# Kernel optimization log

Measured on AMD Instinct MI355X. Metric: run time of the kernel, lower is better.

Reference implementation:

```python
import jax, jax.numpy as jnp
import numpy as np

EPS = 1e-6
NHEADS = 16


def setup_inputs() -> dict:
    key = jax.random.key(0)
    ks = jax.random.split(key, 6)
    b, n, dim, h = 2, 2048, 2048, NHEADS
    d = dim // h
    x = jax.random.normal(ks[0], (b, n, dim), dtype=jnp.float32)
    qkv_w = jax.random.normal(ks[1], (3 * dim, dim), dtype=jnp.float32) * (dim ** -0.5)
    qkv_b = jax.random.normal(ks[2], (3 * dim,), dtype=jnp.float32) * 0.01
    q_norm_w = jnp.ones((d,), dtype=jnp.float32)
    k_norm_w = jnp.ones((d,), dtype=jnp.float32)
    # Flux-style rotation matrices: (1, 1, n, d/2, 2, 2)
    pos = jnp.arange(n, dtype=jnp.float32)[:, None]
    inv_freq = 1.0 / (10000.0 ** (jnp.arange(0, d, 2, dtype=jnp.float32) / d))  # [d/2]
    ang = pos * inv_freq[None, :]  # [n, d/2]
    cos, sin = jnp.cos(ang), jnp.sin(ang)
    rot = jnp.stack([jnp.stack([cos, -sin], axis=-1),
                     jnp.stack([sin, cos], axis=-1)], axis=-1)  # [n, d/2, 2, 2]
    rot = rot[None, None]  # [1,1,n,d/2,2,2]
    return {"x": x, "qkv_w": qkv_w, "qkv_b": qkv_b,
            "q_norm_w": q_norm_w, "k_norm_w": k_norm_w, "rot": rot}


def _rmsnorm(t, w):
    t32 = t.astype(jnp.float32)
    inv = jax.lax.rsqrt(jnp.mean(t32 * t32, axis=-1, keepdims=True) + EPS)
    return ((t32 * inv) * w).astype(t.dtype)


def _apply_rope(t, rot):
    # t: [b,h,n,d]; rot: [1,1,n,d/2,2,2]
    b, h, n, d = t.shape
    tx = t.astype(jnp.float32).reshape(b, h, n, d // 2, 1, 2)
    out = rot[..., 0] * tx[..., 0] + rot[..., 1] * tx[..., 1]  # [b,h,n,d/2,2]
    return out.reshape(b, h, n, d).astype(t.dtype)


def reference(x, qkv_w, qkv_b, q_norm_w, k_norm_w, rot):
    b, n, dim = x.shape
    d = q_norm_w.shape[0]
    h = dim // d
    qkv = x @ qkv_w.T + qkv_b  # [b, n, 3*dim]
    # layout per Rearrange 'b n (h d j) -> b h n d j'
    qkv = qkv.reshape(b, n, h, d, 3).transpose(0, 2, 1, 3, 4)  # [b,h,n,d,3]
    q, k, v = qkv[..., 0], qkv[..., 1], qkv[..., 2]
    q = _apply_rope(_rmsnorm(q, q_norm_w), rot)
    k = _apply_rope(_rmsnorm(k, k_norm_w), rot)
    scores = jnp.einsum('bhqd,bhkd->bhqk', q, k) * (d ** -0.5)
    attn = jax.nn.softmax(scores, axis=-1)
    out = jnp.einsum('bhqk,bhkd->bhqd', attn, v)
    return out.transpose(0, 2, 1, 3).reshape(b, n, dim)  # b n (h d)
```

## Files before the change

kernel.cpp:

```cpp
#include <hip/hip_runtime.h>
#include <cstdint>
#include <cstddef>


#define LOG2E 1.4426950408889634f
#define ATT_SCALE 0.08838834764831845f
#define QSCALE (ATT_SCALE * LOG2E)

typedef __attribute__((ext_vector_type(8))) __bf16 bf16x8;
typedef __attribute__((ext_vector_type(4))) __bf16 bf16x4;
typedef __attribute__((ext_vector_type(4))) float f32x4;

__device__ __forceinline__ float b2f(unsigned u) {
  u <<= 16;
  return __builtin_bit_cast(float, u);
}
__device__ __forceinline__ unsigned short f2b(float f) {
  unsigned x = __builtin_bit_cast(unsigned, f);
  return (unsigned short)((x + 0x7fffu + ((x >> 16) & 1u)) >> 16);
}
__device__ __forceinline__ void gl16(const void* g, void* l) {
  __builtin_amdgcn_global_load_lds((__attribute__((address_space(1))) void*)(g),
                                   (__attribute__((address_space(3))) void*)(l), 16, 0, 0);
}

__global__ void k_cvt(const float4* __restrict__ in, ushort4* __restrict__ out, int n4) {
  int i = blockIdx.x * blockDim.x + threadIdx.x;
  int st = gridDim.x * blockDim.x;
  for (; i < n4; i += st) {
    float4 v = in[i];
    ushort4 o;
    o.x = f2b(v.x); o.y = f2b(v.y); o.z = f2b(v.z); o.w = f2b(v.w);
    out[i] = o;
  }
}

__global__ __launch_bounds__(512, 2) void k_gemm(const unsigned short* __restrict__ A,
                                                 const unsigned short* __restrict__ W,
                                                 const float* __restrict__ bias,
                                                 unsigned short* __restrict__ C) {
  __shared__ __align__(16) unsigned short lds[65536];
  const int tid = threadIdx.x;
  const int w = tid >> 6, l = tid & 63;
  const int lo = l & 15, hi = l >> 4;
  const int WM = w >> 2, WN = w & 3;
  const int wg = blockIdx.x;
  const int swz = (wg & 7) * 64 + (wg >> 3);
  const int mbase = (swz >> 4) * 128, nbase = (swz & 15) * 384;

  const int srow = w * 16 + (l >> 2);
  const int scol = ((l & 3) * 8) ^ (((srow >> 1) & 3) << 3);

  auto stage = [&](int t, int slot) {
    unsigned short* Sa = lds + slot * 16384;
    unsigned short* Sb = Sa + 4096;
    const int kt = t * 32;
    gl16(A + (size_t)(mbase + srow) * 2048 + kt + scol,
         Sa + (w * 16) * 32);
#pragma unroll
    for (int rd = 0; rd < 3; ++rd)
      gl16(W + (size_t)(nbase + rd * 128 + srow) * 2048 + kt + scol,
           Sb + (rd * 128 + w * 16) * 32);
  };

  f32x4 acc[4][6] = {};
  stage(0, 0); stage(1, 1); stage(2, 2);

  const int ea = (hi * 8) ^ (((lo >> 1) & 3) << 3);
  for (int t = 0; t < 64; ++t) {
    if (t < 62)       asm volatile("s_waitcnt vmcnt(8) lgkmcnt(0)" ::: "memory");
    else if (t == 62) asm volatile("s_waitcnt vmcnt(4) lgkmcnt(0)" ::: "memory");
    else              asm volatile("s_waitcnt vmcnt(0) lgkmcnt(0)" ::: "memory");
    __builtin_amdgcn_sched_barrier(0);
    __builtin_amdgcn_s_barrier();
    __builtin_amdgcn_sched_barrier(0);
    if (t + 3 < 64) stage(t + 3, (t + 3) & 3);

    const unsigned short* Sa = lds + (t & 3) * 16384;
    const unsigned short* Sb = Sa + 4096;
    bf16x8 af[4], bf[6];
#pragma unroll
    for (int i = 0; i < 4; ++i)
      af[i] = *(const bf16x8*)&Sa[(WM * 64 + i * 16 + lo) * 32 + ea];
#pragma unroll
    for (int j = 0; j < 6; ++j)
      bf[j] = *(const bf16x8*)&Sb[(WN * 96 + j * 16 + lo) * 32 + ea];

    __builtin_amdgcn_s_setprio(1);
#pragma unroll
    for (int i = 0; i < 4; ++i)
#pragma unroll
      for (int j = 0; j < 6; ++j)
        acc[i][j] = __builtin_amdgcn_mfma_f32_16x16x32_bf16(af[i], bf[j], acc[i][j], 0, 0, 0);
    __builtin_amdgcn_s_setprio(0);
  }

  const int rowb = mbase + WM * 64;
  const int colb = nbase + WN * 96;
#pragma unroll
  for (int j = 0; j < 6; ++j) {
    float bj = bias[colb + j * 16 + lo];
#pragma unroll
    for (int i = 0; i < 4; ++i)
#pragma unroll
      for (int r = 0; r < 4; ++r) {
        int row = rowb + i * 16 + hi * 4 + r;
        C[(size_t)row * 6144 + colb + j * 16 + lo] = f2b(acc[i][j][r] + bj);
      }
  }
}

__global__ __launch_bounds__(256) void k_normrope(const unsigned short* __restrict__ qkv,
                                                  const float* __restrict__ qw,
                                                  const float* __restrict__ kw,
                                                  const float* __restrict__ rot,
                                                  unsigned short* __restrict__ Q,
                                                  unsigned short* __restrict__ K,
                                                  unsigned short* __restrict__ V) {
  const int l = threadIdx.x & 63;
  const int idx = blockIdx.x * 4 + (threadIdx.x >> 6);
  const int h = idx & 15;
  const int n = (idx >> 4) & 2047;
  const int b = idx >> 15;
  const unsigned* p = (const unsigned*)(qkv + (size_t)(b * 2048 + n) * 6144 + h * 384 + l * 6);
  unsigned u0 = p[0], u1 = p[1], u2 = p[2];
  float q0 = b2f(u0 & 0xffff), k0 = b2f(u0 >> 16);
  float v0 = b2f(u1 & 0xffff), q1 = b2f(u1 >> 16);
  float k1 = b2f(u2 & 0xffff), v1 = b2f(u2 >> 16);
  (void)v0; (void)v1;
  float sq = q0 * q0 + q1 * q1, sk = k0 * k0 + k1 * k1;
#pragma unroll
  for (int m = 1; m < 64; m <<= 1) {
    sq += __shfl_xor(sq, m, 64);
    sk += __shfl_xor(sk, m, 64);
  }
  float qi = rsqrtf(sq * (1.0f / 128.0f) + 1e-6f) * QSCALE;
  float ki = rsqrtf(sk * (1.0f / 128.0f) + 1e-6f);
  float2 qwv = *(const float2*)&qw[2 * l];
  float2 kwv = *(const float2*)&kw[2 * l];
  float4 r = *(const float4*)&rot[n * 256 + l * 4];
  float qn0 = q0 * qi * qwv.x, qn1 = q1 * qi * qwv.y;
  float kn0 = k0 * ki * kwv.x, kn1 = k1 * ki * kwv.y;
  unsigned qo = (unsigned)f2b(r.x * qn0 + r.y * qn1) | ((unsigned)f2b(r.z * qn0 + r.w * qn1) << 16);
  unsigned ko = (unsigned)f2b(r.x * kn0 + r.y * kn1) | ((unsigned)f2b(r.z * kn0 + r.w * kn1) << 16);
  unsigned vo = (u1 & 0xffffu) | (u2 & 0xffff0000u);
  size_t ob = ((size_t)(b * 16 + h) * 2048 + n) * 128 + 2 * l;
  *(unsigned*)(Q + ob) = qo;
  *(unsigned*)(K + ob) = ko;
  *(unsigned*)(V + ob) = vo;
}

__global__ __launch_bounds__(256) void k_transpose(const unsigned short* __restrict__ V,
                                                   unsigned short* __restrict__ Vt) {
  __shared__ unsigned short tile[64 * 66];
  const int t = threadIdx.x;
  const int d0 = blockIdx.x * 64;
  const int n0 = blockIdx.y * 64;
  const int bh = blockIdx.z;
#pragma unroll
  for (int s = t; s < 512; s += 256) {
    int nr = s >> 3, c8 = (s & 7) * 8;
    uint4 vv = *(const uint4*)(V + ((size_t)bh * 2048 + n0 + nr) * 128 + d0 + c8);
    unsigned* tp = (unsigned*)&tile[nr * 66 + c8];
    tp[0] = vv.x; tp[1] = vv.y; tp[2] = vv.z; tp[3] = vv.w;
  }
  __syncthreads();
#pragma unroll
  for (int s = t; s < 512; s += 256) {
    int dr = s >> 3, n8 = (s & 7) * 8;
    unsigned short e[8];
#pragma unroll
    for (int j = 0; j < 8; ++j) e[j] = tile[(n8 + j) * 66 + dr];
    uint4 o;
    o.x = e[0] | ((unsigned)e[1] << 16);
    o.y = e[2] | ((unsigned)e[3] << 16);
    o.z = e[4] | ((unsigned)e[5] << 16);
    o.w = e[6] | ((unsigned)e[7] << 16);
    *(uint4*)(Vt + ((size_t)bh * 128 + d0 + dr) * 2048 + n0 + n8) = o;
  }
}

__global__ __launch_bounds__(512, 4) void k_attn(const unsigned short* __restrict__ Q,
                                                 const unsigned short* __restrict__ K,
                                                 const unsigned short* __restrict__ Vt,
                                                 float* __restrict__ out) {
  __shared__ __align__(16) unsigned short lds[40960];
  unsigned short* Ps = lds + 32768;
  const int tid = threadIdx.x;
  const int w = tid >> 6, l = tid & 63;
  const int lo = l & 15, hi = l >> 4;
  const int swz = (lo & 7) << 3;
  const int qt = blockIdx.x, bh = blockIdx.y;
  const unsigned short* Qb = Q + (size_t)bh * 2048 * 128;
  const unsigned short* Kb = K + (size_t)bh * 2048 * 128;
  const unsigned short* Vb = Vt + (size_t)bh * 128 * 2048;
  unsigned short* Psw = Ps + w * 1024;

  bf16x8 qf[4];
  const int qrow = qt * 128 + w * 16 + lo;
#pragma unroll
  for (int dk = 0; dk < 4; ++dk)
    qf[dk] = *(const bf16x8*)&Qb[(size_t)qrow * 128 + dk * 32 + hi * 8];

  f32x4 Oacc[8] = {};
  float m_run = -__builtin_inff(), l_run = 0.0f;

  const int krow0 = w * 4 + hi;
  const int vrow0 = w * 8 + (l >> 3);
  const unsigned short* kp = Kb + (size_t)krow0 * 128 + ((lo * 8) ^ ((krow0 & 7) << 3));
  const unsigned short* vp = Vb + (size_t)vrow0 * 2048 + (((l & 7) * 8) ^ ((vrow0 & 7) << 3));

  auto stage = [&](int t, int b) {
    unsigned short* Ksb = lds + b * 16384;
    unsigned short* Vtsb = Ksb + 8192;
#pragma unroll
    for (int r = 0; r < 2; ++r) {
      gl16(kp + (size_t)t * 8192 + r * 4096,
           Ksb + (r * 32 + w * 4) * 128);
      gl16(vp + (size_t)r * 131072 + t * 64,
           Vtsb + (r * 64 + w * 8) * 64);
    }
  };

  stage(0, 0);
  int cur = 0;
  for (int t = 0; t < 32; ++t) {
    __syncthreads();
    if (t + 1 < 32) stage(t + 1, cur ^ 1);
    const unsigned short* Ks = lds + cur * 16384;
    const unsigned short* Vts = Ks + 8192;

    f32x4 S[4] = {};
#pragma unroll
    for (int kf = 0; kf < 4; ++kf)
#pragma unroll
      for (int dk = 0; dk < 4; ++dk)
        S[kf] = __builtin_amdgcn_mfma_f32_16x16x32_bf16(
            *(const bf16x8*)&Ks[(kf * 16 + lo) * 128 + ((dk * 32 + hi * 8) ^ swz)],
            qf[dk], S[kf], 0, 0, 0);

    float m01, m23, mt;
    m01 = fmaxf(fmaxf(S[0][0], S[0][1]), fmaxf(S[0][2], S[0][3]));
    m23 = fmaxf(fmaxf(S[1][0], S[1][1]), fmaxf(S[1][2], S[1][3]));
    mt = fmaxf(m01, m23);
    m01 = fmaxf(fmaxf(S[2][0], S[2][1]), fmaxf(S[2][2], S[2][3]));
    m23 = fmaxf(fmaxf(S[3][0], S[3][1]), fmaxf(S[3][2], S[3][3]));
    mt = fmaxf(mt, fmaxf(m01, m23));
    mt = fmaxf(mt, __shfl_xor(mt, 16, 64));
    mt = fmaxf(mt, __shfl_xor(mt, 32, 64));

    const bool defer = __all(mt <= m_run + 8.0f);
    float m_new = m_run, alpha = 1.0f;
    if (!defer) {
      m_new = fmaxf(m_run, mt);
      alpha = exp2f(m_run - m_new);
    }

    float p[4][4];
    float ls = 0.0f;
#pragma unroll
    for (int kf = 0; kf < 4; ++kf)
#pragma unroll
      for (int r = 0; r < 4; ++r) {
        p[kf][r] = exp2f(S[kf][r] - m_new);
        ls += p[kf][r];
      }
    ls += __shfl_xor(ls, 16, 64);
    ls += __shfl_xor(ls, 32, 64);

#pragma unroll
    for (int kf = 0; kf < 4; ++kf) {
      bf16x4 pk;
      pk[0] = (__bf16)p[kf][0]; pk[1] = (__bf16)p[kf][1];
      pk[2] = (__bf16)p[kf][2]; pk[3] = (__bf16)p[kf][3];
      *(bf16x4*)&Psw[lo * 64 + ((kf * 16 + hi * 4) ^ swz)] = pk;
    }

    if (!defer) {
#pragma unroll
      for (int df = 0; df < 8; ++df) {
        Oacc[df][0] *= alpha; Oacc[df][1] *= alpha;
        Oacc[df][2] *= alpha; Oacc[df][3] *= alpha;
      }
      l_run = l_run * alpha + ls;
      m_run = m_new;
    } else {
      l_run += ls;
    }

    const bf16x8 pb0 = *(const bf16x8*)&Psw[lo * 64 + ((hi * 8) ^ swz)];
    const bf16x8 pb1 = *(const bf16x8*)&Psw[lo * 64 + ((32 + hi * 8) ^ swz)];
#pragma unroll
    for (int df = 0; df < 8; ++df) {
      Oacc[df] = __builtin_amdgcn_mfma_f32_16x16x32_bf16(
          *(const bf16x8*)&Vts[(df * 16 + lo) * 64 + ((hi * 8) ^ swz)], pb0, Oacc[df], 0, 0, 0);
      Oacc[df] = __builtin_amdgcn_mfma_f32_16x16x32_bf16(
          *(const bf16x8*)&Vts[(df * 16 + lo) * 64 + ((32 + hi * 8) ^ swz)], pb1, Oacc[df], 0, 0, 0);
    }
    cur ^= 1;
  }

  const float inv = 1.0f / l_run;
  __syncthreads();
  float* Ot = ((float*)lds) + w * 2048;
#pragma unroll
  for (int df = 0; df < 8; ++df)
#pragma unroll
    for (int r = 0; r < 4; ++r)
      Ot[lo * 128 + df * 16 + hi * 4 + r] = Oacc[df][r] * inv;
  const int b = bh >> 4, h = bh & 15;
  const int q2 = l >> 2, c = (l & 3) * 32;
  float* op = out + ((size_t)(b * 2048 + qt * 128 + w * 16 + q2) * 2048 + h * 128 + c);
#pragma unroll
  for (int u = 0; u < 8; ++u)
    *(float4*)&op[u * 4] = *(const float4*)&Ot[q2 * 128 + c + u * 4];
}

extern "C" void kernel_launch(void* const* d_in, const int* in_sizes, int n_in,
                              void* d_out, int out_size, void* d_ws, size_t ws_size,
                              hipStream_t stream) {
  (void)in_sizes; (void)n_in; (void)out_size; (void)ws_size;
  const float* x = (const float*)d_in[0];
  const float* qkv_w = (const float*)d_in[1];
  const float* qkv_b = (const float*)d_in[2];
  const float* q_norm_w = (const float*)d_in[3];
  const float* k_norm_w = (const float*)d_in[4];
  const float* rot = (const float*)d_in[5];
  float* out = (float*)d_out;
  char* ws = (char*)d_ws;
  unsigned short* xb  = (unsigned short*)(ws);
  unsigned short* wb  = (unsigned short*)(ws + 16777216);
  unsigned short* qkv = (unsigned short*)(ws + 41943040);
  unsigned short* Qb  = (unsigned short*)(ws + 92274688);
  unsigned short* Kb  = (unsigned short*)(ws + 109051904);
  unsigned short* Vb  = (unsigned short*)(ws + 125829120);
  unsigned short* Vtb = (unsigned short*)(ws);

  hipLaunchKernelGGL(k_cvt, dim3(1024), dim3(256), 0, stream,
                     (const float4*)x, (ushort4*)xb, 8388608 / 4);
  hipLaunchKernelGGL(k_cvt, dim3(1024), dim3(256), 0, stream,
                     (const float4*)qkv_w, (ushort4*)wb, 12582912 / 4);
  hipLaunchKernelGGL(k_gemm, dim3(512), dim3(512), 0, stream, xb, wb, qkv_b, qkv);
  hipLaunchKernelGGL(k_normrope, dim3(16384), dim3(256), 0, stream,
                     qkv, q_norm_w, k_norm_w, rot, Qb, Kb, Vb);
  hipLaunchKernelGGL(k_transpose, dim3(2, 32, 32), dim3(256), 0, stream, Vb, Vtb);
  hipLaunchKernelGGL(k_attn, dim3(16, 32), dim3(512), 0, stream, Qb, Kb, Vtb, out);
}
```

Before: 260.5 us.

## Process two query sub-tiles per wave in attention to reuse K/V fragments

Each wave now handles 32 query rows, as two 16-row sub-tiles with separate softmax state, instead of 16. Each K and V fragment read from LDS therefore feeds two MFMAs, which halves LDS traffic and global K/V staging per query. The grid shrinks to 256 blocks, mapped linearly with a remap so neighbouring blocks cover different heads. Launch bounds drop to 2 blocks per CU to leave room for the doubled register accumulators, which lowers occupancy and leaves fewer blocks than a 256-CU device can balance well.

Result: no change. 265.5 us (+1.9%).

```diff
diff --git a/kernel.cpp b/kernel.cpp
--- a/kernel.cpp
+++ b/kernel.cpp
@@ -180,30 +180,36 @@
   }
 }
 
-__global__ __launch_bounds__(512, 4) void k_attn(const unsigned short* __restrict__ Q,
+__global__ __launch_bounds__(512, 2) void k_attn(const unsigned short* __restrict__ Q,
                                                  const unsigned short* __restrict__ K,
                                                  const unsigned short* __restrict__ Vt,
                                                  float* __restrict__ out) {
-  __shared__ __align__(16) unsigned short lds[40960];
+  __shared__ __align__(16) unsigned short lds[49152];
   unsigned short* Ps = lds + 32768;
   const int tid = threadIdx.x;
   const int w = tid >> 6, l = tid & 63;
   const int lo = l & 15, hi = l >> 4;
   const int swz = (lo & 7) << 3;
-  const int qt = blockIdx.x, bh = blockIdx.y;
+  const int id = blockIdx.x;
+  const int bh = (id & 7) * 4 + ((id >> 3) & 3);
+  const int qt = id >> 5;
   const unsigned short* Qb = Q + (size_t)bh * 2048 * 128;
   const unsigned short* Kb = K + (size_t)bh * 2048 * 128;
   const unsigned short* Vb = Vt + (size_t)bh * 128 * 2048;
-  unsigned short* Psw = Ps + w * 1024;
-
-  bf16x8 qf[4];
-  const int qrow = qt * 128 + w * 16 + lo;
-#pragma unroll
-  for (int dk = 0; dk < 4; ++dk)
-    qf[dk] = *(const bf16x8*)&Qb[(size_t)qrow * 128 + dk * 32 + hi * 8];
-
-  f32x4 Oacc[8] = {};
-  float m_run = -__builtin_inff(), l_run = 0.0f;
+  unsigned short* Pswa = Ps + w * 2048;
+  unsigned short* Pswb = Pswa + 1024;
+
+  bf16x8 qfa[4], qfb[4];
+  const int qrow = qt * 256 + w * 32 + lo;
+#pragma unroll
+  for (int dk = 0; dk < 4; ++dk) {
+    qfa[dk] = *(const bf16x8*)&Qb[(size_t)qrow * 128 + dk * 32 + hi * 8];
+    qfb[dk] = *(const bf16x8*)&Qb[(size_t)(qrow + 16) * 128 + dk * 32 + hi * 8];
+  }
+
+  f32x4 Oa[8] = {}, Ob[8] = {};
+  float m_a = -__builtin_inff(), l_a = 0.0f;
+  float m_b = -__builtin_inff(), l_b = 0.0f;
 
   const int krow0 = w * 4 + hi;
   const int vrow0 = w * 8 + (l >> 3);
@@ -222,23 +228,7 @@
     }
   };
 
-  stage(0, 0);
-  int cur = 0;
-  for (int t = 0; t < 32; ++t) {
-    __syncthreads();
-    if (t + 1 < 32) stage(t + 1, cur ^ 1);
-    const unsigned short* Ks = lds + cur * 16384;
-    const unsigned short* Vts = Ks + 8192;
-
-    f32x4 S[4] = {};
-#pragma unroll
-    for (int kf = 0; kf < 4; ++kf)
-#pragma unroll
-      for (int dk = 0; dk < 4; ++dk)
-        S[kf] = __builtin_amdgcn_mfma_f32_16x16x32_bf16(
-            *(const bf16x8*)&Ks[(kf * 16 + lo) * 128 + ((dk * 32 + hi * 8) ^ swz)],
-            qf[dk], S[kf], 0, 0, 0);
-
+  auto softmax = [&](f32x4* S, float& m_run, float& l_run, unsigned short* Psw_, f32x4* Oacc) {
     float m01, m23, mt;
     m01 = fmaxf(fmaxf(S[0][0], S[0][1]), fmaxf(S[0][2], S[0][3]));
     m23 = fmaxf(fmaxf(S[1][0], S[1][1]), fmaxf(S[1][2], S[1][3]));
@@ -248,14 +238,12 @@
     mt = fmaxf(mt, fmaxf(m01, m23));
     mt = fmaxf(mt, __shfl_xor(mt, 16, 64));
     mt = fmaxf(mt, __shfl_xor(mt, 32, 64));
-
     const bool defer = __all(mt <= m_run + 8.0f);
     float m_new = m_run, alpha = 1.0f;
     if (!defer) {
       m_new = fmaxf(m_run, mt);
       alpha = exp2f(m_run - m_new);
     }
-
     float p[4][4];
     float ls = 0.0f;
 #pragma unroll
@@ -267,15 +255,13 @@
       }
     ls += __shfl_xor(ls, 16, 64);
     ls += __shfl_xor(ls, 32, 64);
-
 #pragma unroll
     for (int kf = 0; kf < 4; ++kf) {
       bf16x4 pk;
       pk[0] = (__bf16)p[kf][0]; pk[1] = (__bf16)p[kf][1];
       pk[2] = (__bf16)p[kf][2]; pk[3] = (__bf16)p[kf][3];
-      *(bf16x4*)&Psw[lo * 64 + ((kf * 16 + hi * 4) ^ swz)] = pk;
-    }
-
+      *(bf16x4*)&Psw_[lo * 64 + ((kf * 16 + hi * 4) ^ swz)] = pk;
+    }
     if (!defer) {
 #pragma unroll
       for (int df = 0; df < 8; ++df) {
@@ -287,33 +273,78 @@
     } else {
       l_run += ls;
     }
-
-    const bf16x8 pb0 = *(const bf16x8*)&Psw[lo * 64 + ((hi * 8) ^ swz)];
-    const bf16x8 pb1 = *(const bf16x8*)&Psw[lo * 64 + ((32 + hi * 8) ^ swz)];
+  };
+
+  stage(0, 0);
+  int cur = 0;
+  for (int t = 0; t < 32; ++t) {
+    __syncthreads();
+    if (t + 1 < 32) stage(t + 1, cur ^ 1);
+    const unsigned short* Ks = lds + cur * 16384;
+    const unsigned short* Vts = Ks + 8192;
+
+    f32x4 Sa[4] = {}, Sb[4] = {};
+#pragma unroll
+    for (int kf = 0; kf < 4; ++kf)
+#pragma unroll
+      for (int dk = 0; dk < 4; ++dk) {
+        const bf16x8 kfrag =
+            *(const bf16x8*)&Ks[(kf * 16 + lo) * 128 + ((dk * 32 + hi * 8) ^ swz)];
+        Sa[kf] = __builtin_amdgcn_mfma_f32_16x16x32_bf16(kfrag, qfa[dk], Sa[kf], 0, 0, 0);
+        Sb[kf] = __builtin_amdgcn_mfma_f32_16x16x32_bf16(kfrag, qfb[dk], Sb[kf], 0, 0, 0);
+      }
+
+    softmax(Sa, m_a, l_a, Pswa, Oa);
+    softmax(Sb, m_b, l_b, Pswb, Ob);
+
+    const bf16x8 pa0 = *(const bf16x8*)&Pswa[lo * 64 + ((hi * 8) ^ swz)];
+    const bf16x8 pa1 = *(const bf16x8*)&Pswa[lo * 64 + ((32 + hi * 8) ^ swz)];
+    const bf16x8 pb0 = *(const bf16x8*)&Pswb[lo * 64 + ((hi * 8) ^ swz)];
+    const bf16x8 pb1 = *(const bf16x8*)&Pswb[lo * 64 + ((32 + hi * 8) ^ swz)];
 #pragma unroll
     for (int df = 0; df < 8; ++df) {
-      Oacc[df] = __builtin_amdgcn_mfma_f32_16x16x32_bf16(
-          *(const bf16x8*)&Vts[(df * 16 + lo) * 64 + ((hi * 8) ^ swz)], pb0, Oacc[df], 0, 0, 0);
-      Oacc[df] = __builtin_amdgcn_mfma_f32_16x16x32_bf16(
-          *(const bf16x8*)&Vts[(df * 16 + lo) * 64 + ((32 + hi * 8) ^ swz)], pb1, Oacc[df], 0, 0, 0);
+      const bf16x8 v0 = *(const bf16x8*)&Vts[(df * 16 + lo) * 64 + ((hi * 8) ^ swz)];
+      const bf16x8 v1 = *(const bf16x8*)&Vts[(df * 16 + lo) * 64 + ((32 + hi * 8) ^ swz)];
+      Oa[df] = __builtin_amdgcn_mfma_f32_16x16x32_bf16(v0, pa0, Oa[df], 0, 0, 0);
+      Oa[df] = __builtin_amdgcn_mfma_f32_16x16x32_bf16(v1, pa1, Oa[df], 0, 0, 0);
+      Ob[df] = __builtin_amdgcn_mfma_f32_16x16x32_bf16(v0, pb0, Ob[df], 0, 0, 0);
+      Ob[df] = __builtin_amdgcn_mfma_f32_16x16x32_bf16(v1, pb1, Ob[df], 0, 0, 0);
     }
     cur ^= 1;
   }
 
-  const float inv = 1.0f / l_run;
-  __syncthreads();
-  float* Ot = ((float*)lds) + w * 2048;
-#pragma unroll
-  for (int df = 0; df < 8; ++df)
-#pragma unroll
-    for (int r = 0; r < 4; ++r)
-      Ot[lo * 128 + df * 16 + hi * 4 + r] = Oacc[df][r] * inv;
+  const float inva = 1.0f / l_a;
+  const float invb = 1.0f / l_b;
   const int b = bh >> 4, h = bh & 15;
   const int q2 = l >> 2, c = (l & 3) * 32;
-  float* op = out + ((size_t)(b * 2048 + qt * 128 + w * 16 + q2) * 2048 + h * 128 + c);
-#pragma unroll
-  for (int u = 0; u < 8; ++u)
-    *(float4*)&op[u * 4] = *(const float4*)&Ot[q2 * 128 + c + u * 4];
+  float* Ot = ((float*)lds) + w * 2048;
+
+  __syncthreads();
+#pragma unroll
+  for (int df = 0; df < 8; ++df)
+#pragma unroll
+    for (int r = 0; r < 4; ++r)
+      Ot[lo * 128 + df * 16 + hi * 4 + r] = Oa[df][r] * inva;
+  __syncthreads();
+  {
+    float* op = out + ((size_t)(b * 2048 + qt * 256 + w * 32 + q2) * 2048 + h * 128 + c);
+#pragma unroll
+    for (int u = 0; u < 8; ++u)
+      *(float4*)&op[u * 4] = *(const float4*)&Ot[q2 * 128 + c + u * 4];
+  }
+  __syncthreads();
+#pragma unroll
+  for (int df = 0; df < 8; ++df)
+#pragma unroll
+    for (int r = 0; r < 4; ++r)
+      Ot[lo * 128 + df * 16 + hi * 4 + r] = Ob[df][r] * invb;
+  __syncthreads();
+  {
+    float* op = out + ((size_t)(b * 2048 + qt * 256 + w * 32 + 16 + q2) * 2048 + h * 128 + c);
+#pragma unroll
+    for (int u = 0; u < 8; ++u)
+      *(float4*)&op[u * 4] = *(const float4*)&Ot[q2 * 128 + c + u * 4];
+  }
 }
 
 extern "C" void kernel_launch(void* const* d_in, const int* in_sizes, int n_in,
@@ -344,5 +375,5 @@
   hipLaunchKernelGGL(k_normrope, dim3(16384), dim3(256), 0, stream,
                      qkv, q_norm_w, k_norm_w, rot, Qb, Kb, Vb);
   hipLaunchKernelGGL(k_transpose, dim3(2, 32, 32), dim3(256), 0, stream, Vb, Vtb);
-  hipLaunchKernelGGL(k_attn, dim3(16, 32), dim3(512), 0, stream, Qb, Kb, Vtb, out);
-}
+  hipLaunchKernelGGL(k_attn, dim3(256), dim3(512), 0, stream, Qb, Kb, Vtb, out);
+}
```
